# Kernel optimization log

Measured on AMD Instinct MI355X. Metric: run time of the kernel, lower is better.

## Reference

```python
import jax, jax.numpy as jnp
import numpy as np

B, T, M, D = 4, 512, 16, 128
P, H = 128, 4
E = P // H


def _glorot(k, shape, fan_in, fan_out):
    lim = np.sqrt(6.0 / (fan_in + fan_out)).astype(np.float32)
    return jax.random.uniform(k, shape, jnp.float32, -lim, lim)


def setup_inputs() -> dict:
    key = jax.random.key(0)
    ks = jax.random.split(key, 12)
    inp = jax.random.normal(ks[0], (B, T, M, D), jnp.float32)
    pos = jax.random.normal(ks[1], (B, T, 1, D), jnp.float32)
    # padding mask: valid time steps per batch element (ensures no fully-masked softmax row)
    lengths = jax.random.randint(ks[2], (B,), T // 2, T + 1)
    mask = jnp.broadcast_to(jnp.arange(T)[None, :, None] < lengths[:, None, None], (B, T, M))
    Wq = _glorot(ks[3], (M, P, D), D, P)
    Wk = _glorot(ks[4], (M, P, D), D, P)
    Wv = _glorot(ks[5], (M, P, D), D, P)
    Wq_t = _glorot(ks[6], (M, P, D), D, P)
    Wk_t = _glorot(ks[7], (M, P, D), D, P)
    Bq = jnp.zeros((M, P), jnp.float32)
    Bk = jnp.zeros((M, P), jnp.float32)
    Bv = jnp.zeros((M, P), jnp.float32)
    Bq_t = jnp.zeros((M, P), jnp.float32)
    Bk_t = jnp.zeros((M, P), jnp.float32)
    return {"inp": inp, "pos": pos, "mask": mask,
            "Wq": Wq, "Bq": Bq, "Wk": Wk, "Bk": Bk, "Wv": Wv, "Bv": Bv,
            "Wq_t": Wq_t, "Bq_t": Bq_t, "Wk_t": Wk_t, "Bk_t": Bk_t}


def reference(inp, pos, mask, Wq, Bq, Wk, Bk, Wv, Bv, Wq_t, Bq_t, Wk_t, Bk_t):
    b, t, m, d = inp.shape
    p = Wq.shape[1]
    h, e = H, P // H
    # per-modality projections: (m,p,d) x (b,t,m,d) -> (b,t,m,p)
    q = jnp.einsum('mpd,btmd->btmp', Wq, inp) + Bq
    k = jnp.einsum('mpd,btmd->btmp', Wk, inp) + Bk
    v = jnp.einsum('mpd,btmd->btmp', Wv, inp) + Bv
    pos0 = pos[:, :, 0, :]  # (b,t,d); broadcasts across m
    q_t = jnp.einsum('mpd,btd->btmp', Wq_t, pos0) + Bq_t
    k_t = jnp.einsum('mpd,btd->btmp', Wk_t, pos0) + Bk_t

    def split_heads(x):  # (b,t,m,p) -> (b,m,h,t,e)
        return x.reshape(b, t, m, h, e).transpose(0, 2, 3, 1, 4)

    q, k, v, q_t, k_t = map(split_heads, (q, k, v, q_t, k_t))
    # dual bilinear score: content + positional
    score = (jnp.einsum('bmhte,bmhse->bmhts', q, k)
             + jnp.einsum('bmhte,bmhse->bmhts', q_t, k_t)) / (2.0 * np.sqrt(e).astype(np.float32))
    causal = jnp.tril(jnp.ones((t, t), bool))  # (t,t)
    score = jnp.where(causal, score, -jnp.inf)
    km = mask.transpose(0, 2, 1)[:, :, None, None, :]  # (b,m,1,1,t)
    score = jnp.where(km, score, -jnp.inf)
    w = jax.nn.softmax(score, axis=-1)
    w = jnp.where(km, w, 0.0)
    w = jnp.where(causal, w, 0.0)
    # dropout is identity at inference (drop_rate ignored)
    out = jnp.einsum('bmhts,bmhse->bmhte', w, v)
    return out.transpose(0, 3, 1, 2, 4).reshape(b, t, m, p)
```

## Files before the change

kernel.cpp:

```cpp
#include <hip/hip_runtime.h>

#define Bn 4
#define Tn 512
#define Mn 16
#define Dn 128
#define Pn 128
#define Hn 4
#define En 32
#define SCALE 0.08838834764831845f

typedef unsigned short u16;
typedef unsigned int u32;
typedef short s16;
typedef __attribute__((ext_vector_type(8))) s16 bf16x8;
typedef __attribute__((ext_vector_type(4))) float f32x4;

__device__ __forceinline__ u16 f2b(float f) {
  u32 x; __builtin_memcpy(&x, &f, 4);
  x += 0x7fffu + ((x >> 16) & 1u);
  return (u16)(x >> 16);
}
__device__ __forceinline__ bf16x8 ld8(const u16* p) {
  bf16x8 r; __builtin_memcpy(&r, p, 16); return r;
}
__device__ __forceinline__ f32x4 mfma16(bf16x8 a, bf16x8 b, f32x4 c) {
  return __builtin_amdgcn_mfma_f32_16x16x32_bf16(a, b, c, 0, 0, 0);
}

__global__ void lengths_kernel(const void* __restrict__ mask, int* __restrict__ len_out) {
  const int b = blockIdx.x;
  __shared__ int cnt[256];
  const u32 w0 = ((const u32*)mask)[0];
  const int mode = (w0 == 1u) ? 0 : (w0 == 0x3F800000u) ? 1
                 : (w0 == 0x3F803F80u) ? 2 : 3;
  int c = 0;
  for (int t = threadIdx.x; t < Tn; t += 256) {
    const size_t idx = ((size_t)b * Tn + t) * Mn;
    int nz;
    if (mode == 0)      nz = (((const int*)mask)[idx] != 0);
    else if (mode == 1) nz = (((const u32*)mask)[idx] != 0u);
    else if (mode == 2) nz = (((const u16*)mask)[idx] != 0);
    else                nz = (((const unsigned char*)mask)[idx] != 0);
    c += nz;
  }
  cnt[threadIdx.x] = c;
  __syncthreads();
  for (int s = 128; s > 0; s >>= 1) {
    if (threadIdx.x < (unsigned)s) cnt[threadIdx.x] += cnt[threadIdx.x + s];
    __syncthreads();
  }
  if (threadIdx.x == 0) len_out[b] = cnt[0];
}

__global__ __launch_bounds__(256) void proj_mfma(
    const float* __restrict__ inp, const float* __restrict__ pos,
    const float* __restrict__ Wq, const float* __restrict__ Bq,
    const float* __restrict__ Wk, const float* __restrict__ Bk,
    const float* __restrict__ Wv, const float* __restrict__ Bv,
    const float* __restrict__ Wqt, const float* __restrict__ Bqt,
    const float* __restrict__ Wkt, const float* __restrict__ Bkt,
    u16* __restrict__ Qh, u16* __restrict__ Kh, u16* __restrict__ Vh) {
  const int tid = threadIdx.x;
  const int bid = blockIdx.x;
  const int tsel = bid % 5;
  const int m = (bid / 5) % Mn;
  const int rt0 = (bid / (5 * Mn)) * 128;

  const float* W; const float* Bb; int usepos, doscale;
  switch (tsel) {
    case 0:  W = Wq;  Bb = Bq;  usepos = 0; doscale = 1; break;
    case 1:  W = Wk;  Bb = Bk;  usepos = 0; doscale = 0; break;
    case 2:  W = Wv;  Bb = Bv;  usepos = 0; doscale = 0; break;
    case 3:  W = Wqt; Bb = Bqt; usepos = 1; doscale = 1; break;
    default: W = Wkt; Bb = Bkt; usepos = 1; doscale = 0; break;
  }
  const float* A = usepos ? pos : inp;

  __shared__ __align__(16) u16 Xs[128 * 136];
  __shared__ __align__(16) u16 Ws[128 * 136];

  for (int idx = tid; idx < 128 * 32; idx += 256) {
    const int row = idx >> 5, c4 = (idx & 31) * 4;
    const size_t src = usepos ? ((size_t)(rt0 + row) * Dn + c4)
                              : (((size_t)(rt0 + row) * Mn + m) * Dn + c4);
    const float4 x = *(const float4*)(A + src);
    ushort4 xh; xh.x = f2b(x.x); xh.y = f2b(x.y); xh.z = f2b(x.z); xh.w = f2b(x.w);
    *(ushort4*)&Xs[row * 136 + c4] = xh;
    const float4 w = *(const float4*)(W + ((size_t)m * Pn + row) * Dn + c4);
    ushort4 wh; wh.x = f2b(w.x); wh.y = f2b(w.y); wh.z = f2b(w.z); wh.w = f2b(w.w);
    *(ushort4*)&Ws[row * 136 + c4] = wh;
  }
  __syncthreads();

  const int wv = tid >> 6, lane = tid & 63;
  const int quad = lane >> 4, l16 = lane & 15;

  f32x4 acc[2][8];
#pragma unroll
  for (int qs = 0; qs < 2; ++qs)
#pragma unroll
    for (int n = 0; n < 8; ++n) acc[qs][n] = (f32x4){0.f, 0.f, 0.f, 0.f};

#pragma unroll
  for (int kc = 0; kc < 4; ++kc) {
    const int ko = kc * 32 + quad * 8;
    const bf16x8 a0 = ld8(&Xs[(wv * 32 + l16) * 136 + ko]);
    const bf16x8 a1 = ld8(&Xs[(wv * 32 + 16 + l16) * 136 + ko]);
#pragma unroll
    for (int n = 0; n < 8; ++n) {
      const bf16x8 bn = ld8(&Ws[(n * 16 + l16) * 136 + ko]);
      acc[0][n] = mfma16(a0, bn, acc[0][n]);
      acc[1][n] = mfma16(a1, bn, acc[1][n]);
    }
  }

  u16* dst = (tsel == 2) ? Vh : ((tsel == 0 || tsel == 3) ? Qh : Kh);
  const int coloff = (tsel >= 3) ? 32 : 0;
  const int ostride = (tsel == 2) ? 32 : 64;
#pragma unroll
  for (int n = 0; n < 8; ++n) {
    const int p = n * 16 + l16;
    const float bias = Bb[m * Pn + p];
    const int hh = p >> 5, e = p & 31;
#pragma unroll
    for (int qs = 0; qs < 2; ++qs)
#pragma unroll
      for (int reg = 0; reg < 4; ++reg) {
        const int r = rt0 + wv * 32 + qs * 16 + quad * 4 + reg;
        float v = acc[qs][n][reg] + bias;
        if (doscale) v *= SCALE;
        const int b = r >> 9, t = r & (Tn - 1);
        const size_t ob = (((size_t)b * Mn + m) * Hn + hh) * Tn + t;
        dst[ob * ostride + coloff + e] = f2b(v);
      }
  }
}

__global__ __launch_bounds__(256) void attn_mfma(
    const u16* __restrict__ Qh, const u16* __restrict__ Kh,
    const u16* __restrict__ Vh, const int* __restrict__ lens,
    float* __restrict__ out) {
  const int bid = blockIdx.x;
  const int qt = bid & 3;
  const int h = (bid >> 2) & (Hn - 1);
  const int m = (bid >> 4) & (Mn - 1);
  const int b = bid >> 8;
  const int len = lens[b];
  const int qt0 = qt * 128;

  __shared__ __align__(16) u16 Ks[128 * 72];
  __shared__ __align__(16) u16 Vt[32 * 136];
  __shared__ __align__(16) u16 Ps[128 * 136];

  const int tid = threadIdx.x;
  const int wv = tid >> 6, lane = tid & 63;
  const int quad = lane >> 4, l16 = lane & 15;
  const size_t base = (((size_t)b * Mn + m) * Hn + h) * Tn;

  bf16x8 aq[2][2];
#pragma unroll
  for (int qs = 0; qs < 2; ++qs)
#pragma unroll
    for (int kc = 0; kc < 2; ++kc)
      aq[qs][kc] = ld8(Qh + (base + qt0 + wv * 32 + qs * 16 + l16) * 64 + kc * 32 + quad * 8);

  f32x4 O[2][2];
#pragma unroll
  for (int qs = 0; qs < 2; ++qs)
#pragma unroll
    for (int es = 0; es < 2; ++es) O[qs][es] = (f32x4){0.f, 0.f, 0.f, 0.f};
  float mr[2][4], lr[2][4];
#pragma unroll
  for (int qs = 0; qs < 2; ++qs)
#pragma unroll
    for (int reg = 0; reg < 4; ++reg) { mr[qs][reg] = -1e30f; lr[qs][reg] = 0.f; }

  const int s_hi = min(qt0 + 128, len);
  for (int s0 = 0; s0 < s_hi; s0 += 128) {
    for (int idx = tid; idx < 128 * 8; idx += 256) {
      const int row = idx >> 3, c8 = (idx & 7) * 8;
      const uint4 u = *(const uint4*)(Kh + (base + s0 + row) * 64 + c8);
      *(uint4*)&Ks[row * 72 + c8] = u;
    }
    for (int idx = tid; idx < 128 * 4; idx += 256) {
      const int row = idx >> 2, c8 = (idx & 3) * 8;
      const uint4 u = *(const uint4*)(Vh + (base + s0 + row) * 32 + c8);
      const u16* us = (const u16*)&u;
#pragma unroll
      for (int j = 0; j < 8; ++j) Vt[(c8 + j) * 136 + row] = us[j];
    }
    __syncthreads();

    f32x4 S[2][8];
#pragma unroll
    for (int qs = 0; qs < 2; ++qs)
#pragma unroll
      for (int st = 0; st < 8; ++st) S[qs][st] = (f32x4){0.f, 0.f, 0.f, 0.f};
#pragma unroll
    for (int kc = 0; kc < 2; ++kc) {
      const int ko = kc * 32 + quad * 8;
#pragma unroll
      for (int st = 0; st < 8; ++st) {
        const bf16x8 bk = ld8(&Ks[(st * 16 + l16) * 72 + ko]);
        S[0][st] = mfma16(aq[0][kc], bk, S[0][st]);
        S[1][st] = mfma16(aq[1][kc], bk, S[1][st]);
      }
    }

#pragma unroll
    for (int qs = 0; qs < 2; ++qs) {
#pragma unroll
      for (int reg = 0; reg < 4; ++reg) {
        const int q = qt0 + wv * 32 + qs * 16 + quad * 4 + reg;
        float cmax = -1e30f;
#pragma unroll
        for (int st = 0; st < 8; ++st) {
          const int s = s0 + st * 16 + l16;
          if ((s <= q) && (s < len)) cmax = fmaxf(cmax, S[qs][st][reg]);
        }
        cmax = fmaxf(cmax, __shfl_xor(cmax, 1));
        cmax = fmaxf(cmax, __shfl_xor(cmax, 2));
        cmax = fmaxf(cmax, __shfl_xor(cmax, 4));
        cmax = fmaxf(cmax, __shfl_xor(cmax, 8));
        const float mold = mr[qs][reg];
        const float mnew = fmaxf(mold, cmax);
        const float alpha = __expf(mold - mnew);
        float rsum = 0.f;
#pragma unroll
        for (int st = 0; st < 8; ++st) {
          const int s = s0 + st * 16 + l16;
          const float p = ((s <= q) && (s < len)) ? __expf(S[qs][st][reg] - mnew) : 0.f;
          rsum += p;
          Ps[(wv * 32 + qs * 16 + quad * 4 + reg) * 136 + st * 16 + l16] = f2b(p);
        }
        rsum += __shfl_xor(rsum, 1);
        rsum += __shfl_xor(rsum, 2);
        rsum += __shfl_xor(rsum, 4);
        rsum += __shfl_xor(rsum, 8);
        lr[qs][reg] = lr[qs][reg] * alpha + rsum;
        mr[qs][reg] = mnew;
#pragma unroll
        for (int es = 0; es < 2; ++es) O[qs][es][reg] *= alpha;
      }
    }
    __syncthreads();

#pragma unroll
    for (int kc = 0; kc < 4; ++kc) {
      const int ko = kc * 32 + quad * 8;
#pragma unroll
      for (int qs = 0; qs < 2; ++qs) {
        const bf16x8 ap = ld8(&Ps[(wv * 32 + qs * 16 + l16) * 136 + ko]);
#pragma unroll
        for (int es = 0; es < 2; ++es) {
          const bf16x8 bv = ld8(&Vt[(es * 16 + l16) * 136 + ko]);
          O[qs][es] = mfma16(ap, bv, O[qs][es]);
        }
      }
    }
    __syncthreads();
  }

#pragma unroll
  for (int qs = 0; qs < 2; ++qs)
#pragma unroll
    for (int reg = 0; reg < 4; ++reg) {
      const int t = qt0 + wv * 32 + qs * 16 + quad * 4 + reg;
      const float linv = 1.0f / lr[qs][reg];
#pragma unroll
      for (int es = 0; es < 2; ++es)
        out[(((size_t)b * Tn + t) * Mn + m) * Pn + h * En + es * 16 + l16] =
            O[qs][es][reg] * linv;
    }
}

extern "C" void kernel_launch(void* const* d_in, const int* in_sizes, int n_in,
                              void* d_out, int out_size, void* d_ws, size_t ws_size,
                              hipStream_t stream) {
  const float* inp = (const float*)d_in[0];
  const float* pos = (const float*)d_in[1];
  const void* mask = d_in[2];
  const float* Wq  = (const float*)d_in[3];
  const float* Bq  = (const float*)d_in[4];
  const float* Wk  = (const float*)d_in[5];
  const float* Bk  = (const float*)d_in[6];
  const float* Wv  = (const float*)d_in[7];
  const float* Bv  = (const float*)d_in[8];
  const float* Wqt = (const float*)d_in[9];
  const float* Bqt = (const float*)d_in[10];
  const float* Wkt = (const float*)d_in[11];
  const float* Bkt = (const float*)d_in[12];
  float* out = (float*)d_out;

  const size_t nQ = (size_t)Bn * Mn * Hn * Tn * 64;
  const size_t nV = (size_t)Bn * Mn * Hn * Tn * 32;
  u16* Qh = (u16*)d_ws;
  u16* Kh = Qh + nQ;
  u16* Vh = Kh + nQ;
  int* lens = (int*)(Vh + nV);

  lengths_kernel<<<Bn, 256, 0, stream>>>(mask, lens);
  proj_mfma<<<(Bn * Tn / 128) * Mn * 5, 256, 0, stream>>>(
      inp, pos, Wq, Bq, Wk, Bk, Wv, Bv, Wqt, Bqt, Wkt, Bkt, Qh, Kh, Vh);
  attn_mfma<<<Bn * Mn * Hn * (Tn / 128), 256, 0, stream>>>(Qh, Kh, Vh, lens, out);
}
```

Baseline: 168.4 us.

## Restructure attention into per-wave flash tiles with transposed V and split Q/K buffers

```diff
diff --git a/kernel.cpp b/kernel.cpp
--- a/kernel.cpp
+++ b/kernel.cpp
@@ -6,7 +6,6 @@
 #define Dn 128
 #define Pn 128
 #define Hn 4
-#define En 32
 #define SCALE 0.08838834764831845f
 
 typedef unsigned short u16;
@@ -19,6 +18,9 @@
   u32 x; __builtin_memcpy(&x, &f, 4);
   x += 0x7fffu + ((x >> 16) & 1u);
   return (u16)(x >> 16);
+}
+__device__ __forceinline__ u32 pack2(float a, float b) {
+  return (u32)f2b(a) | ((u32)f2b(b) << 16);
 }
 __device__ __forceinline__ bf16x8 ld8(const u16* p) {
   bf16x8 r; __builtin_memcpy(&r, p, 16); return r;
@@ -59,7 +61,8 @@
     const float* __restrict__ Wv, const float* __restrict__ Bv,
     const float* __restrict__ Wqt, const float* __restrict__ Bqt,
     const float* __restrict__ Wkt, const float* __restrict__ Bkt,
-    u16* __restrict__ Qh, u16* __restrict__ Kh, u16* __restrict__ Vh) {
+    u16* __restrict__ Qa, u16* __restrict__ Ka, u16* __restrict__ Qb,
+    u16* __restrict__ Kb, u16* __restrict__ Vt) {
   const int tid = threadIdx.x;
   const int bid = blockIdx.x;
   const int tsel = bid % 5;
@@ -67,30 +70,18 @@
   const int rt0 = (bid / (5 * Mn)) * 128;
 
   const float* W; const float* Bb; int usepos, doscale;
+  u16* dst;
   switch (tsel) {
-    case 0:  W = Wq;  Bb = Bq;  usepos = 0; doscale = 1; break;
-    case 1:  W = Wk;  Bb = Bk;  usepos = 0; doscale = 0; break;
-    case 2:  W = Wv;  Bb = Bv;  usepos = 0; doscale = 0; break;
-    case 3:  W = Wqt; Bb = Bqt; usepos = 1; doscale = 1; break;
-    default: W = Wkt; Bb = Bkt; usepos = 1; doscale = 0; break;
+    case 0:  W = Wq;  Bb = Bq;  usepos = 0; doscale = 1; dst = Qa; break;
+    case 1:  W = Wk;  Bb = Bk;  usepos = 0; doscale = 0; dst = Ka; break;
+    case 2:  W = Wv;  Bb = Bv;  usepos = 0; doscale = 0; dst = Vt; break;
+    case 3:  W = Wqt; Bb = Bqt; usepos = 1; doscale = 1; dst = Qb; break;
+    default: W = Wkt; Bb = Bkt; usepos = 1; doscale = 0; dst = Kb; break;
   }
   const float* A = usepos ? pos : inp;
 
-  __shared__ __align__(16) u16 Xs[128 * 136];
-  __shared__ __align__(16) u16 Ws[128 * 136];
-
-  for (int idx = tid; idx < 128 * 32; idx += 256) {
-    const int row = idx >> 5, c4 = (idx & 31) * 4;
-    const size_t src = usepos ? ((size_t)(rt0 + row) * Dn + c4)
-                              : (((size_t)(rt0 + row) * Mn + m) * Dn + c4);
-    const float4 x = *(const float4*)(A + src);
-    ushort4 xh; xh.x = f2b(x.x); xh.y = f2b(x.y); xh.z = f2b(x.z); xh.w = f2b(x.w);
-    *(ushort4*)&Xs[row * 136 + c4] = xh;
-    const float4 w = *(const float4*)(W + ((size_t)m * Pn + row) * Dn + c4);
-    ushort4 wh; wh.x = f2b(w.x); wh.y = f2b(w.y); wh.z = f2b(w.z); wh.w = f2b(w.w);
-    *(ushort4*)&Ws[row * 136 + c4] = wh;
-  }
-  __syncthreads();
+  __shared__ __align__(16) u16 Xs[128 * 72];
+  __shared__ __align__(16) u16 Ws2[128 * 72];
 
   const int wv = tid >> 6, lane = tid & 63;
   const int quad = lane >> 4, l16 = lane & 15;
@@ -101,177 +92,191 @@
 #pragma unroll
     for (int n = 0; n < 8; ++n) acc[qs][n] = (f32x4){0.f, 0.f, 0.f, 0.f};
 
-#pragma unroll
-  for (int kc = 0; kc < 4; ++kc) {
-    const int ko = kc * 32 + quad * 8;
-    const bf16x8 a0 = ld8(&Xs[(wv * 32 + l16) * 136 + ko]);
-    const bf16x8 a1 = ld8(&Xs[(wv * 32 + 16 + l16) * 136 + ko]);
-#pragma unroll
-    for (int n = 0; n < 8; ++n) {
-      const bf16x8 bn = ld8(&Ws[(n * 16 + l16) * 136 + ko]);
-      acc[0][n] = mfma16(a0, bn, acc[0][n]);
-      acc[1][n] = mfma16(a1, bn, acc[1][n]);
-    }
-  }
-
-  u16* dst = (tsel == 2) ? Vh : ((tsel == 0 || tsel == 3) ? Qh : Kh);
-  const int coloff = (tsel >= 3) ? 32 : 0;
-  const int ostride = (tsel == 2) ? 32 : 64;
+  for (int kh = 0; kh < 2; ++kh) {
+    for (int idx = tid; idx < 128 * 16; idx += 256) {
+      const int row = idx >> 4, c4 = (idx & 15) * 4, col = kh * 64 + c4;
+      const size_t sx = usepos ? ((size_t)(rt0 + row) * Dn + col)
+                               : (((size_t)(rt0 + row) * Mn + m) * Dn + col);
+      const float4 x = *(const float4*)(A + sx);
+      ushort4 xh; xh.x = f2b(x.x); xh.y = f2b(x.y); xh.z = f2b(x.z); xh.w = f2b(x.w);
+      *(ushort4*)&Xs[row * 72 + c4] = xh;
+      const float4 w = *(const float4*)(W + ((size_t)m * Pn + row) * Dn + col);
+      ushort4 wh; wh.x = f2b(w.x); wh.y = f2b(w.y); wh.z = f2b(w.z); wh.w = f2b(w.w);
+      *(ushort4*)&Ws2[row * 72 + c4] = wh;
+    }
+    __syncthreads();
+#pragma unroll
+    for (int kc = 0; kc < 2; ++kc) {
+      const int ko = kc * 32 + quad * 8;
+      const bf16x8 a0 = ld8(&Xs[(wv * 32 + l16) * 72 + ko]);
+      const bf16x8 a1 = ld8(&Xs[(wv * 32 + 16 + l16) * 72 + ko]);
+#pragma unroll
+      for (int n = 0; n < 8; ++n) {
+        const bf16x8 bn = ld8(&Ws2[(n * 16 + l16) * 72 + ko]);
+        acc[0][n] = mfma16(a0, bn, acc[0][n]);
+        acc[1][n] = mfma16(a1, bn, acc[1][n]);
+      }
+    }
+    __syncthreads();
+  }
+
+  const int b = rt0 >> 9;
+  const int tl0 = (rt0 & (Tn - 1)) + wv * 32;
 #pragma unroll
   for (int n = 0; n < 8; ++n) {
-    const int p = n * 16 + l16;
-    const float bias = Bb[m * Pn + p];
-    const int hh = p >> 5, e = p & 31;
-#pragma unroll
-    for (int qs = 0; qs < 2; ++qs)
-#pragma unroll
-      for (int reg = 0; reg < 4; ++reg) {
-        const int r = rt0 + wv * 32 + qs * 16 + quad * 4 + reg;
-        float v = acc[qs][n][reg] + bias;
-        if (doscale) v *= SCALE;
-        const int b = r >> 9, t = r & (Tn - 1);
-        const size_t ob = (((size_t)b * Mn + m) * Hn + hh) * Tn + t;
-        dst[ob * ostride + coloff + e] = f2b(v);
+    const int h = n >> 1, e = (n & 1) * 16 + l16;
+    const float bias = Bb[m * Pn + n * 16 + l16];
+    const int bmh = (b * Mn + m) * Hn + h;
+    if (tsel != 2) {
+#pragma unroll
+      for (int qs = 0; qs < 2; ++qs)
+#pragma unroll
+        for (int reg = 0; reg < 4; ++reg) {
+          const int t = tl0 + qs * 16 + quad * 4 + reg;
+          float v = acc[qs][n][reg] + bias;
+          if (doscale) v *= SCALE;
+          dst[((size_t)bmh * Tn + t) * 32 + e] = f2b(v);
+        }
+    } else {
+      const size_t rowv = ((size_t)bmh * 32 + e) * Tn;
+#pragma unroll
+      for (int qs = 0; qs < 2; ++qs) {
+        const int t0 = tl0 + qs * 16 + quad * 4;
+        uint2 d;
+        d.x = pack2(acc[qs][n][0] + bias, acc[qs][n][1] + bias);
+        d.y = pack2(acc[qs][n][2] + bias, acc[qs][n][3] + bias);
+        *(uint2*)&dst[rowv + t0] = d;
       }
-  }
-}
-
-__global__ __launch_bounds__(256) void attn_mfma(
-    const u16* __restrict__ Qh, const u16* __restrict__ Kh,
-    const u16* __restrict__ Vh, const int* __restrict__ lens,
+    }
+  }
+}
+
+__global__ __launch_bounds__(256, 4) void attn_flash(
+    const u16* __restrict__ Qa, const u16* __restrict__ Ka,
+    const u16* __restrict__ Qb, const u16* __restrict__ Kb,
+    const u16* __restrict__ Vt, const int* __restrict__ lens,
     float* __restrict__ out) {
-  const int bid = blockIdx.x;
-  const int qt = bid & 3;
-  const int h = (bid >> 2) & (Hn - 1);
-  const int m = (bid >> 4) & (Mn - 1);
-  const int b = bid >> 8;
-  const int len = lens[b];
-  const int qt0 = qt * 128;
-
-  __shared__ __align__(16) u16 Ks[128 * 72];
-  __shared__ __align__(16) u16 Vt[32 * 136];
-  __shared__ __align__(16) u16 Ps[128 * 136];
+  __shared__ __align__(16) u16 Ps[4 * 32 * 72];
 
   const int tid = threadIdx.x;
   const int wv = tid >> 6, lane = tid & 63;
   const int quad = lane >> 4, l16 = lane & 15;
-  const size_t base = (((size_t)b * Mn + m) * Hn + h) * Tn;
-
-  bf16x8 aq[2][2];
+
+  const int wu = blockIdx.x * 4 + wv;
+  const int qt = wu & 15;
+  const int bmh = wu >> 4;
+  const int b = bmh >> 6;
+  const int len = lens[b];
+  const int q0 = qt * 32;
+
+  const size_t rowbase = (size_t)bmh * Tn;
+  const size_t vbase = (size_t)bmh * 32 * Tn;
+  u16* myPs = &Ps[wv * 32 * 72];
+
+  bf16x8 qf[2][2];
+#pragma unroll
+  for (int qs = 0; qs < 2; ++qs) {
+    const size_t r = (rowbase + q0 + qs * 16 + l16) * 32 + quad * 8;
+    qf[qs][0] = ld8(Qa + r);
+    qf[qs][1] = ld8(Qb + r);
+  }
+
+  f32x4 O[2][2];
 #pragma unroll
   for (int qs = 0; qs < 2; ++qs)
 #pragma unroll
-    for (int kc = 0; kc < 2; ++kc)
-      aq[qs][kc] = ld8(Qh + (base + qt0 + wv * 32 + qs * 16 + l16) * 64 + kc * 32 + quad * 8);
-
-  f32x4 O[2][2];
-#pragma unroll
-  for (int qs = 0; qs < 2; ++qs)
-#pragma unroll
     for (int es = 0; es < 2; ++es) O[qs][es] = (f32x4){0.f, 0.f, 0.f, 0.f};
-  float mr[2][4], lr[2][4];
-#pragma unroll
-  for (int qs = 0; qs < 2; ++qs)
-#pragma unroll
-    for (int reg = 0; reg < 4; ++reg) { mr[qs][reg] = -1e30f; lr[qs][reg] = 0.f; }
-
-  const int s_hi = min(qt0 + 128, len);
-  for (int s0 = 0; s0 < s_hi; s0 += 128) {
-    for (int idx = tid; idx < 128 * 8; idx += 256) {
-      const int row = idx >> 3, c8 = (idx & 7) * 8;
-      const uint4 u = *(const uint4*)(Kh + (base + s0 + row) * 64 + c8);
-      *(uint4*)&Ks[row * 72 + c8] = u;
-    }
-    for (int idx = tid; idx < 128 * 4; idx += 256) {
-      const int row = idx >> 2, c8 = (idx & 3) * 8;
-      const uint4 u = *(const uint4*)(Vh + (base + s0 + row) * 32 + c8);
-      const u16* us = (const u16*)&u;
-#pragma unroll
-      for (int j = 0; j < 8; ++j) Vt[(c8 + j) * 136 + row] = us[j];
-    }
-    __syncthreads();
-
-    f32x4 S[2][8];
-#pragma unroll
-    for (int qs = 0; qs < 2; ++qs)
-#pragma unroll
-      for (int st = 0; st < 8; ++st) S[qs][st] = (f32x4){0.f, 0.f, 0.f, 0.f};
+  float mrow[2] = {-1e30f, -1e30f}, lsum[2] = {0.f, 0.f};
+
+  const int s_hi = min(q0 + 32, len);
+  for (int s0 = 0; s0 < s_hi; s0 += 64) {
+    f32x4 S[2][4];
+#pragma unroll
+    for (int st = 0; st < 4; ++st) {
+      const size_t kr = (rowbase + s0 + st * 16 + l16) * 32 + quad * 8;
+      const bf16x8 k0 = ld8(Ka + kr);
+      const bf16x8 k1 = ld8(Kb + kr);
+#pragma unroll
+      for (int qs = 0; qs < 2; ++qs)
+        S[qs][st] = mfma16(k1, qf[qs][1], mfma16(k0, qf[qs][0],
+                           st == -1 ? S[qs][st] : (f32x4){0.f, 0.f, 0.f, 0.f}));
+    }
+
+#pragma unroll
+    for (int qs = 0; qs < 2; ++qs) {
+      const int q = q0 + qs * 16 + l16;
+      const int qcap = min(q, len - 1);
+      const int sb = s0 + quad * 4;
+      float cmax = -1e30f;
+#pragma unroll
+      for (int st = 0; st < 4; ++st)
+#pragma unroll
+        for (int reg = 0; reg < 4; ++reg) {
+          const int s = sb + st * 16 + reg;
+          const float v = (s <= qcap) ? S[qs][st][reg] : -1e30f;
+          S[qs][st][reg] = v;
+          cmax = fmaxf(cmax, v);
+        }
+      cmax = fmaxf(cmax, __shfl_xor(cmax, 16));
+      cmax = fmaxf(cmax, __shfl_xor(cmax, 32));
+      const float mnew = fmaxf(mrow[qs], cmax);
+      const float alpha = __expf(mrow[qs] - mnew);
+      mrow[qs] = mnew;
+      float rsum = 0.f;
+      u32 pk[4][2];
+#pragma unroll
+      for (int st = 0; st < 4; ++st) {
+        const float p0 = __expf(S[qs][st][0] - mnew);
+        const float p1 = __expf(S[qs][st][1] - mnew);
+        const float p2 = __expf(S[qs][st][2] - mnew);
+        const float p3 = __expf(S[qs][st][3] - mnew);
+        rsum += (p0 + p1) + (p2 + p3);
+        pk[st][0] = pack2(p0, p1);
+        pk[st][1] = pack2(p2, p3);
+      }
+      rsum += __shfl_xor(rsum, 16);
+      rsum += __shfl_xor(rsum, 32);
+      lsum[qs] = lsum[qs] * alpha + rsum;
+#pragma unroll
+      for (int es = 0; es < 2; ++es)
+#pragma unroll
+        for (int reg = 0; reg < 4; ++reg) O[qs][es][reg] *= alpha;
+#pragma unroll
+      for (int st = 0; st < 4; ++st) {
+        uint2 d; d.x = pk[st][0]; d.y = pk[st][1];
+        *(uint2*)&myPs[(qs * 16 + l16) * 72 + st * 16 + quad * 4] = d;
+      }
+    }
+
 #pragma unroll
     for (int kc = 0; kc < 2; ++kc) {
       const int ko = kc * 32 + quad * 8;
-#pragma unroll
-      for (int st = 0; st < 8; ++st) {
-        const bf16x8 bk = ld8(&Ks[(st * 16 + l16) * 72 + ko]);
-        S[0][st] = mfma16(aq[0][kc], bk, S[0][st]);
-        S[1][st] = mfma16(aq[1][kc], bk, S[1][st]);
-      }
-    }
-
-#pragma unroll
-    for (int qs = 0; qs < 2; ++qs) {
-#pragma unroll
-      for (int reg = 0; reg < 4; ++reg) {
-        const int q = qt0 + wv * 32 + qs * 16 + quad * 4 + reg;
-        float cmax = -1e30f;
-#pragma unroll
-        for (int st = 0; st < 8; ++st) {
-          const int s = s0 + st * 16 + l16;
-          if ((s <= q) && (s < len)) cmax = fmaxf(cmax, S[qs][st][reg]);
-        }
-        cmax = fmaxf(cmax, __shfl_xor(cmax, 1));
-        cmax = fmaxf(cmax, __shfl_xor(cmax, 2));
-        cmax = fmaxf(cmax, __shfl_xor(cmax, 4));
-        cmax = fmaxf(cmax, __shfl_xor(cmax, 8));
-        const float mold = mr[qs][reg];
-        const float mnew = fmaxf(mold, cmax);
-        const float alpha = __expf(mold - mnew);
-        float rsum = 0.f;
-#pragma unroll
-        for (int st = 0; st < 8; ++st) {
-          const int s = s0 + st * 16 + l16;
-          const float p = ((s <= q) && (s < len)) ? __expf(S[qs][st][reg] - mnew) : 0.f;
-          rsum += p;
-          Ps[(wv * 32 + qs * 16 + quad * 4 + reg) * 136 + st * 16 + l16] = f2b(p);
-        }
-        rsum += __shfl_xor(rsum, 1);
-        rsum += __shfl_xor(rsum, 2);
-        rsum += __shfl_xor(rsum, 4);
-        rsum += __shfl_xor(rsum, 8);
-        lr[qs][reg] = lr[qs][reg] * alpha + rsum;
-        mr[qs][reg] = mnew;
-#pragma unroll
-        for (int es = 0; es < 2; ++es) O[qs][es][reg] *= alpha;
-      }
-    }
-    __syncthreads();
-
-#pragma unroll
-    for (int kc = 0; kc < 4; ++kc) {
-      const int ko = kc * 32 + quad * 8;
-#pragma unroll
-      for (int qs = 0; qs < 2; ++qs) {
-        const bf16x8 ap = ld8(&Ps[(wv * 32 + qs * 16 + l16) * 136 + ko]);
-#pragma unroll
-        for (int es = 0; es < 2; ++es) {
-          const bf16x8 bv = ld8(&Vt[(es * 16 + l16) * 136 + ko]);
-          O[qs][es] = mfma16(ap, bv, O[qs][es]);
-        }
-      }
-    }
-    __syncthreads();
-  }
-
-#pragma unroll
-  for (int qs = 0; qs < 2; ++qs)
-#pragma unroll
-    for (int reg = 0; reg < 4; ++reg) {
-      const int t = qt0 + wv * 32 + qs * 16 + quad * 4 + reg;
-      const float linv = 1.0f / lr[qs][reg];
-#pragma unroll
-      for (int es = 0; es < 2; ++es)
-        out[(((size_t)b * Tn + t) * Mn + m) * Pn + h * En + es * 16 + l16] =
-            O[qs][es][reg] * linv;
-    }
+      const bf16x8 pf0 = ld8(&myPs[l16 * 72 + ko]);
+      const bf16x8 pf1 = ld8(&myPs[(16 + l16) * 72 + ko]);
+      const bf16x8 vf0 = ld8(Vt + vbase + (size_t)l16 * Tn + s0 + ko);
+      const bf16x8 vf1 = ld8(Vt + vbase + (size_t)(16 + l16) * Tn + s0 + ko);
+      O[0][0] = mfma16(vf0, pf0, O[0][0]);
+      O[0][1] = mfma16(vf1, pf0, O[0][1]);
+      O[1][0] = mfma16(vf0, pf1, O[1][0]);
+      O[1][1] = mfma16(vf1, pf1, O[1][1]);
+    }
+  }
+
+  const int mm = (bmh >> 2) & (Mn - 1);
+  const int h = bmh & (Hn - 1);
+#pragma unroll
+  for (int qs = 0; qs < 2; ++qs) {
+    const float linv = 1.0f / lsum[qs];
+    const int t = q0 + qs * 16 + l16;
+    const size_t ob = (((size_t)b * Tn + t) * Mn + mm) * Pn + h * 32 + quad * 4;
+#pragma unroll
+    for (int es = 0; es < 2; ++es) {
+      float4 o;
+      o.x = O[qs][es][0] * linv; o.y = O[qs][es][1] * linv;
+      o.z = O[qs][es][2] * linv; o.w = O[qs][es][3] * linv;
+      *(float4*)&out[ob + es * 16] = o;
+    }
+  }
 }
 
 extern "C" void kernel_launch(void* const* d_in, const int* in_sizes, int n_in,
@@ -292,15 +297,17 @@
   const float* Bkt = (const float*)d_in[12];
   float* out = (float*)d_out;
 
-  const size_t nQ = (size_t)Bn * Mn * Hn * Tn * 64;
-  const size_t nV = (size_t)Bn * Mn * Hn * Tn * 32;
-  u16* Qh = (u16*)d_ws;
-  u16* Kh = Qh + nQ;
-  u16* Vh = Kh + nQ;
-  int* lens = (int*)(Vh + nV);
+  const size_t nA = (size_t)Bn * Mn * Hn * Tn * 32;
+  u16* Qa = (u16*)d_ws;
+  u16* Ka = Qa + nA;
+  u16* Qb = Ka + nA;
+  u16* Kb = Qb + nA;
+  u16* Vt = Kb + nA;
+  int* lens = (int*)(Vt + nA);
 
   lengths_kernel<<<Bn, 256, 0, stream>>>(mask, lens);
   proj_mfma<<<(Bn * Tn / 128) * Mn * 5, 256, 0, stream>>>(
-      inp, pos, Wq, Bq, Wk, Bk, Wv, Bv, Wqt, Bqt, Wkt, Bkt, Qh, Kh, Vh);
-  attn_mfma<<<Bn * Mn * Hn * (Tn / 128), 256, 0, stream>>>(Qh, Kh, Vh, lens, out);
-}
+      inp, pos, Wq, Bq, Wk, Bk, Wv, Bv, Wqt, Bqt, Wkt, Bkt, Qa, Ka, Qb, Kb, Vt);
+  attn_flash<<<Bn * Mn * Hn * (Tn / 32) / 4, 256, 0, stream>>>(
+      Qa, Ka, Qb, Kb, Vt, lens, out);
+}
```

Measured after the change: 151.3 us. 1.11x faster.
